# Performance work log

Hardware: AMD Instinct MI355X
Metric: run time of the kernel (lower is better)

Reference implementation:

```python
import jax, jax.numpy as jnp
import numpy as np

NEG_SLOPE = 0.2  # PyG GATConv default negative_slope
HEADS1, HID = 8, 256


def gat_conv(x, src, dst, W, att_src, att_dst, bias, heads, out_ch):
    """PyG-style GATConv: project, per-edge attention, segment softmax over dst, scatter-add."""
    N = x.shape[0]
    h = (x @ W.T).reshape(N, heads, out_ch)                 # [N,H,C]
    a_s = jnp.einsum('nhc,hc->nh', h, att_src)              # [N,H]
    a_d = jnp.einsum('nhc,hc->nh', h, att_dst)
    e = jax.nn.leaky_relu(a_s[src] + a_d[dst], NEG_SLOPE)   # [E,H]
    m = jax.ops.segment_max(e, dst, num_segments=N)         # stable softmax per dst node
    ex = jnp.exp(e - m[dst])
    denom = jax.ops.segment_sum(ex, dst, num_segments=N)
    alpha = ex / (denom[dst] + 1e-16)                       # [E,H]
    out = jax.ops.segment_sum(alpha[:, :, None] * h[src], dst, num_segments=N)  # [N,H,C]
    return out.reshape(N, heads * out_ch) + bias


def setup_inputs() -> dict:
    key = jax.random.key(0)
    ks = jax.random.split(key, 20)
    Nc, Ncol, E = 4000, 16000, 100000
    nf, cf, gain, hid, H, emb = 64, 128, 2, HID, HEADS1, 128
    s = 0.05
    return {
        'constraints_state': jax.random.normal(ks[0], (Nc, nf), jnp.float32),
        'columns_state':     jax.random.normal(ks[1], (Ncol, cf), jnp.float32),
        'edges':             jax.random.randint(ks[2], (2, E), 0, Nc + Ncol, jnp.int64),
        'W_node': jax.random.normal(ks[3], (hid, nf * gain), jnp.float32) * s,
        'b_node': jnp.zeros((hid,), jnp.float32),
        'W_col':  jax.random.normal(ks[4], (hid, cf * gain), jnp.float32) * s,
        'b_col':  jnp.zeros((hid,), jnp.float32),
        'W1':       jax.random.normal(ks[5], (H * hid, hid), jnp.float32) * s,
        'att_src1': jax.random.normal(ks[6], (H, hid), jnp.float32) * s,
        'att_dst1': jax.random.normal(ks[7], (H, hid), jnp.float32) * s,
        'b1':       jnp.zeros((H * hid,), jnp.float32),
        'W2':       jax.random.normal(ks[8], (hid, H * hid), jnp.float32) * s,
        'att_src2': jax.random.normal(ks[9], (1, hid), jnp.float32) * s,
        'att_dst2': jax.random.normal(ks[10], (1, hid), jnp.float32) * s,
        'b2':       jnp.zeros((hid,), jnp.float32),
        'W_out': jax.random.normal(ks[11], (emb, hid), jnp.float32) * s,
        'b_out': jnp.zeros((emb,), jnp.float32),
    }


def reference(constraints_state, columns_state, edges,
              W_node, b_node, W_col, b_col,
              W1, att_src1, att_dst1, b1,
              W2, att_src2, att_dst2, b2,
              W_out, b_out):
    gain = 2
    x_n = jnp.tile(constraints_state, (1, gain))
    x_c = jnp.tile(columns_state, (1, gain))
    h_n = jax.nn.relu(x_n @ W_node.T + b_node)
    h_c = jax.nn.relu(x_c @ W_col.T + b_col)
    x = jnp.concatenate([h_n, h_c], axis=0)                 # [N, hid]
    N = x.shape[0]
    loops = jnp.arange(N)
    # conv1: edges as given (+ self-loops, PyG default)
    src1 = jnp.concatenate([edges[0], loops])
    dst1 = jnp.concatenate([edges[1], loops])
    x = jax.nn.relu(gat_conv(x, src1, dst1, W1, att_src1, att_dst1, b1, HEADS1, HID))
    # conv2: flipped edges (+ self-loops), 1 head
    src2 = jnp.concatenate([edges[1], loops])
    dst2 = jnp.concatenate([edges[0], loops])
    x = jax.nn.relu(gat_conv(x, src2, dst2, W2, att_src2, att_dst2, b2, 1, HID))
    logits = x[-columns_state.shape[0]:] @ W_out.T + b_out  # [Ncol, embed_dim]
    return logits
```

## Files before the change

### kernel.cpp

```cpp
#include <hip/hip_runtime.h>


#define NEG_SLOPE 0.2f

typedef __attribute__((ext_vector_type(8))) short bf16x8;
typedef __attribute__((ext_vector_type(4))) float f32x4;

__device__ __forceinline__ float bf2f(unsigned short u) {
  return __uint_as_float(((unsigned)u) << 16);
}
__device__ __forceinline__ unsigned short f2bf(float f) {
  unsigned u = __float_as_uint(f);
  u += 0x7fffu + ((u >> 16) & 1u);
  return (unsigned short)(u >> 16);
}

__device__ __forceinline__ void async_copy16(const void* g, void* l) {
  __builtin_amdgcn_global_load_lds(
      (const __attribute__((address_space(1))) unsigned int*)g,
      (__attribute__((address_space(3))) unsigned int*)l, 16, 0, 0);
}

__global__ void prep(const float* __restrict__ Wn, const float* __restrict__ Wc,
                     const float* __restrict__ W1, const float* __restrict__ W2,
                     const float* __restrict__ Wout,
                     const float* __restrict__ cons, const float* __restrict__ cols,
                     const float* __restrict__ att_s1, const float* __restrict__ att_d1,
                     unsigned short* __restrict__ Wn_b, unsigned short* __restrict__ Wc_b,
                     unsigned short* __restrict__ W1b, unsigned short* __restrict__ W2b,
                     unsigned short* __restrict__ Woutb,
                     unsigned short* __restrict__ consb, unsigned short* __restrict__ colsb,
                     float* __restrict__ v_s1, float* __restrict__ v_d1,
                     int n_cons, int n_cols) {
  const int S0 = 256 * 64;
  const int S1 = 256 * 128;
  const int S2 = 2048 * 256;
  const int S3 = 256 * 2048;
  const int S4 = 128 * 256;
  const int S5 = 2048;
  int total = S0 + S1 + S2 + S3 + S4 + n_cons + n_cols + S5;
  for (int idx = blockIdx.x * 256 + threadIdx.x; idx < total; idx += gridDim.x * 256) {
    int i = idx;
    if (i < S0) { int o = i >> 6, j = i & 63;
      Wn_b[i] = f2bf(Wn[o * 128 + j] + Wn[o * 128 + 64 + j]); continue; }
    i -= S0;
    if (i < S1) { int o = i >> 7, j = i & 127;
      Wc_b[i] = f2bf(Wc[o * 256 + j] + Wc[o * 256 + 128 + j]); continue; }
    i -= S1;
    if (i < S2) { W1b[i] = f2bf(W1[i]); continue; }
    i -= S2;
    if (i < S3) { W2b[i] = f2bf(W2[i]); continue; }
    i -= S3;
    if (i < S4) { Woutb[i] = f2bf(Wout[i]); continue; }
    i -= S4;
    if (i < n_cons) { consb[i] = f2bf(cons[i]); continue; }
    i -= n_cons;
    if (i < n_cols) { colsb[i] = f2bf(cols[i]); continue; }
    i -= n_cols;
    {
      int h = i >> 8, k = i & 255;
      const float* Wrow = W1 + (size_t)h * 256 * 256 + k;
      const float* as = att_s1 + h * 256;
      const float* ad = att_d1 + h * 256;
      float s = 0.f, d = 0.f;
      for (int c = 0; c < 256; ++c) {
        float w = Wrow[(size_t)c * 256];
        s += as[c] * w;
        d += ad[c] * w;
      }
      v_s1[i] = s; v_d1[i] = d;
    }
  }
}

__global__ __launch_bounds__(256) void a1_dots(const unsigned short* __restrict__ xb,
                                               const float* __restrict__ v_s,
                                               const float* __restrict__ v_d,
                                               float* __restrict__ a_s,
                                               float* __restrict__ a_d, int N) {
  __shared__ float vs[2048], vd[2048];
  for (int i = threadIdx.x; i < 2048; i += 256) { vs[i] = v_s[i]; vd[i] = v_d[i]; }
  __syncthreads();
  int n = blockIdx.x * 256 + threadIdx.x;
  if (n >= N) return;
  const unsigned short* row = xb + (size_t)n * 256;
  float s[8] = {}, d[8] = {};
  for (int c = 0; c < 256; c += 8) {
    bf16x8 xv = *(const bf16x8*)(row + c);
    float xf[8];
#pragma unroll
    for (int i = 0; i < 8; ++i) xf[i] = bf2f(((const unsigned short*)&xv)[i]);
#pragma unroll
    for (int h = 0; h < 8; ++h)
#pragma unroll
      for (int i = 0; i < 8; ++i) {
        s[h] += xf[i] * vs[h * 256 + c + i];
        d[h] += xf[i] * vd[h * 256 + c + i];
      }
  }
#pragma unroll
  for (int h = 0; h < 8; ++h) { a_s[n * 8 + h] = s[h]; a_d[n * 8 + h] = d[h]; }
}

template <bool C_BF16, bool BIAS, bool RELU, bool BDIAG>
__global__ __launch_bounds__(512) void gemm_mfma_bt(const unsigned short* __restrict__ A,
                                                    const unsigned short* __restrict__ W,
                                                    const float* __restrict__ bias,
                                                    void* __restrict__ Cv,
                                                    int M, int K, int Nout, int lda) {
  __shared__ short smem[2 * 128 * 64];
  short* sA = smem;
  short* sB = smem + 128 * 64;
  float* Cf = (float*)Cv;
  unsigned short* Cb = (unsigned short*)Cv;

  const int tid = threadIdx.x;
  const int lane = tid & 63, w = tid >> 6;
  const int m0 = blockIdx.y * 128, n0 = blockIdx.x * 128;
  const int koff = BDIAG ? (n0 >> 8) << 8 : 0;
  const int wm = (w & 3) * 32, wn = (w >> 2) * 64;
  const int fr = lane & 15;
  const int frs = fr & 7;
  const int quad = lane >> 4;

  f32x4 acc[2][4];
#pragma unroll
  for (int i = 0; i < 2; ++i)
#pragma unroll
    for (int j = 0; j < 4; ++j) acc[i][j] = (f32x4){0.f, 0.f, 0.f, 0.f};

  for (int k0 = 0; k0 < K; k0 += 64) {
#pragma unroll
    for (int i = 0; i < 2; ++i) {
      int c = i * 512 + tid;
      int row = c >> 3, kc = c & 7;
      int kcs = kc ^ (row & 7);
      int grow = m0 + row;
      if (grow >= M) grow = M - 1;
      async_copy16(A + (size_t)grow * lda + koff + k0 + kcs * 8, &sA[(i * 512 + w * 64) * 8]);
    }
#pragma unroll
    for (int i = 0; i < 2; ++i) {
      int c = i * 512 + tid;
      int row = c >> 3, kc = c & 7;
      int kcs = kc ^ (row & 7);
      async_copy16(W + (size_t)(n0 + row) * K + k0 + kcs * 8, &sB[(i * 512 + w * 64) * 8]);
    }
    __syncthreads();

#pragma unroll
    for (int ks = 0; ks < 2; ++ks) {
      bf16x8 af[2], bfr[4];
#pragma unroll
      for (int mi = 0; mi < 2; ++mi) {
        int row = wm + mi * 16 + fr;
        af[mi] = *(const bf16x8*)&sA[(row * 8 + ((ks * 4 + quad) ^ frs)) * 8];
      }
#pragma unroll
      for (int ni = 0; ni < 4; ++ni) {
        int row = wn + ni * 16 + fr;
        bfr[ni] = *(const bf16x8*)&sB[(row * 8 + ((ks * 4 + quad) ^ frs)) * 8];
      }
#pragma unroll
      for (int mi = 0; mi < 2; ++mi)
#pragma unroll
        for (int ni = 0; ni < 4; ++ni)
          acc[mi][ni] = __builtin_amdgcn_mfma_f32_16x16x32_bf16(
              af[mi], bfr[ni], acc[mi][ni], 0, 0, 0);
    }
    __syncthreads();
  }

  if (C_BF16) {
    unsigned short* hsh = (unsigned short*)smem;
#pragma unroll
    for (int mi = 0; mi < 2; ++mi)
#pragma unroll
      for (int ni = 0; ni < 4; ++ni) {
        int col = wn + ni * 16 + fr;
        float bv = BIAS ? bias[n0 + col] : 0.f;
        f32x4 v = acc[mi][ni];
#pragma unroll
        for (int r = 0; r < 4; ++r) {
          int row = wm + mi * 16 + quad * 4 + r;
          float x = v[r] + bv;
          if (RELU) x = fmaxf(x, 0.f);
          hsh[row * 128 + (col ^ (((row >> 2) & 3) << 5))] = f2bf(x);
        }
      }
    __syncthreads();
#pragma unroll
    for (int i = 0; i < 4; ++i) {
      int slot = i * 512 + tid;
      int row = slot >> 4, cg = slot & 15;
      int colbase = cg * 8;
      bf16x8 val = *(const bf16x8*)&hsh[row * 128 + (colbase ^ (((row >> 2) & 3) << 5))];
      int grow = m0 + row;
      if (grow < M)
        *(bf16x8*)(Cb + (size_t)grow * Nout + n0 + colbase) = val;
    }
  } else {
#pragma unroll
    for (int mi = 0; mi < 2; ++mi)
#pragma unroll
      for (int ni = 0; ni < 4; ++ni) {
        int col = n0 + wn + ni * 16 + fr;
        float bv = BIAS ? bias[col] : 0.f;
        f32x4 v = acc[mi][ni];
#pragma unroll
        for (int r = 0; r < 4; ++r) {
          int row = m0 + wm + mi * 16 + quad * 4 + r;
          if (row < M) {
            float x = v[r] + bv;
            if (RELU) x = fmaxf(x, 0.f);
            Cf[(size_t)row * Nout + col] = x;
          }
        }
      }
  }
}

__global__ __launch_bounds__(512) void gemm_mfma_k2048(const unsigned short* __restrict__ A,
                                                       const unsigned short* __restrict__ W,
                                                       unsigned short* __restrict__ C,
                                                       const float* __restrict__ att_s,
                                                       const float* __restrict__ att_d,
                                                       float* __restrict__ a_s,
                                                       float* __restrict__ a_d,
                                                       int M, int K) {
  __shared__ short sA[32 * 64];
  __shared__ short sB[256 * 64];
  const int tid = threadIdx.x;
  const int lane = tid & 63, w = tid >> 6;
  const int m0 = blockIdx.x * 32;
  const int fr = lane & 15, quad = lane >> 4;
  const int frs = fr & 7;

  f32x4 acc[2][2];
#pragma unroll
  for (int i = 0; i < 2; ++i)
#pragma unroll
    for (int j = 0; j < 2; ++j) acc[i][j] = (f32x4){0.f, 0.f, 0.f, 0.f};

  for (int k0 = 0; k0 < K; k0 += 64) {
    if (w < 4) {
      int row = tid >> 3, kc = tid & 7;
      int kcs = kc ^ (row & 7);
      int grow = m0 + row;
      if (grow >= M) grow = M - 1;
      async_copy16(A + (size_t)grow * K + k0 + kcs * 8, &sA[(w * 64) * 8]);
    }
#pragma unroll
    for (int i = 0; i < 4; ++i) {
      int c = i * 512 + tid;
      int row = c >> 3, kc = c & 7;
      int kcs = kc ^ (row & 7);
      async_copy16(W + (size_t)row * K + k0 + kcs * 8, &sB[(i * 512 + w * 64) * 8]);
    }
    __syncthreads();

#pragma unroll
    for (int ks = 0; ks < 2; ++ks) {
      bf16x8 af[2], bfr[2];
#pragma unroll
      for (int mi = 0; mi < 2; ++mi) {
        int row = mi * 16 + fr;
        af[mi] = *(const bf16x8*)&sA[(row * 8 + ((ks * 4 + quad) ^ frs)) * 8];
      }
#pragma unroll
      for (int ni = 0; ni < 2; ++ni) {
        int row = w * 32 + ni * 16 + fr;
        bfr[ni] = *(const bf16x8*)&sB[(row * 8 + ((ks * 4 + quad) ^ frs)) * 8];
      }
#pragma unroll
      for (int mi = 0; mi < 2; ++mi)
#pragma unroll
        for (int ni = 0; ni < 2; ++ni)
          acc[mi][ni] = __builtin_amdgcn_mfma_f32_16x16x32_bf16(
              af[mi], bfr[ni], acc[mi][ni], 0, 0, 0);
    }
    __syncthreads();
  }

  unsigned short* hsh = (unsigned short*)sB;
#pragma unroll
  for (int mi = 0; mi < 2; ++mi)
#pragma unroll
    for (int ni = 0; ni < 2; ++ni) {
      int col = w * 32 + ni * 16 + fr;
      f32x4 v = acc[mi][ni];
#pragma unroll
      for (int r = 0; r < 4; ++r) {
        int rl = mi * 16 + quad * 4 + r;
        hsh[rl * 256 + col] = f2bf(v[r]);
      }
    }
  __syncthreads();

#pragma unroll
  for (int i = 0; i < 2; ++i) {
    int slot = i * 512 + tid;
    int row = slot >> 5, cg = slot & 31;
    int grow = m0 + row;
    if (grow < M)
      *(bf16x8*)(C + (size_t)grow * 256 + cg * 8) = *(const bf16x8*)&hsh[row * 256 + cg * 8];
  }

  int r = tid >> 4;
  int cbase = (tid & 15) * 16;
  float s = 0.f, d = 0.f;
#pragma unroll
  for (int q = 0; q < 2; ++q) {
    bf16x8 hv8 = *(const bf16x8*)&hsh[r * 256 + cbase + q * 8];
    const unsigned short* hp = (const unsigned short*)&hv8;
#pragma unroll
    for (int i = 0; i < 8; ++i) {
      int c = cbase + q * 8 + i;
      float hv = bf2f(hp[i]);
      s += hv * att_s[c];
      d += hv * att_d[c];
    }
  }
#pragma unroll
  for (int off = 8; off; off >>= 1) {
    s += __shfl_down(s, off);
    d += __shfl_down(d, off);
  }
  if ((tid & 15) == 0 && m0 + r < M) {
    a_s[m0 + r] = s;
    a_d[m0 + r] = d;
  }
}

__global__ void build_count(const void* __restrict__ edges_raw, int E, int N,
                            int* __restrict__ esrc, int* __restrict__ edst,
                            int* __restrict__ cnt1, int* __restrict__ cnt2, int E1) {
  const long long* p64 = (const long long*)edges_raw;
  const int* p32 = (const int*)edges_raw;
  bool is64 = true;
#pragma unroll
  for (int i = 0; i < 8; ++i) {
    long long v = p64[i];
    if (v < 0 || v >= N) is64 = false;
  }
  int idx = blockIdx.x * 256 + threadIdx.x;
  if (idx >= E1) return;
  int s, d;
  if (idx < E) {
    if (is64) { s = (int)p64[idx]; d = (int)p64[E + idx]; }
    else      { s = p32[idx];      d = p32[E + idx]; }
  } else {
    s = d = idx - E;
  }
  esrc[idx] = s;
  edst[idx] = d;
  atomicAdd(&cnt1[d], 1);
  atomicAdd(&cnt2[s], 1);
}

__device__ __forceinline__ void scan_one(const int* __restrict__ cnt,
                                         int* __restrict__ indptr,
                                         int* __restrict__ cur, int N, int* buf) {
  int t = threadIdx.x, lane = t & 63, w = t >> 6;
  int running = 0;
  for (int base = 0; base < N; base += 1024) {
    int v = (base + t < N) ? cnt[base + t] : 0;
    int incl = v;
#pragma unroll
    for (int off = 1; off < 64; off <<= 1) {
      int y = __shfl_up(incl, off);
      if (lane >= off) incl += y;
    }
    if (lane == 63) buf[w] = incl;
    __syncthreads();
    if (t < 16) {
      int x = buf[t];
#pragma unroll
      for (int off = 1; off < 16; off <<= 1) {
        int y = __shfl_up(x, off);
        if (t >= off) x += y;
      }
      buf[t] = x;
    }
    __syncthreads();
    int woff = w ? buf[w - 1] : 0;
    int tot = buf[15];
    if (base + t < N) {
      int excl = running + woff + incl - v;
      indptr[base + t] = excl;
      cur[base + t] = excl;
    }
    running += tot;
    __syncthreads();
  }
  if (t == 0) indptr[N] = running;
  __syncthreads();
}

__global__ __launch_bounds__(1024) void scan2_kernel(const int* cnt1, int* indptr1, int* cur1,
                                                     const int* cnt2, int* indptr2, int* cur2,
                                                     int N) {
  __shared__ int buf[16];
  scan_one(cnt1, indptr1, cur1, N, buf);
  scan_one(cnt2, indptr2, cur2, N, buf);
}

__global__ void scatter_edges(const int* __restrict__ esrc, const int* __restrict__ edst,
                              int* __restrict__ cur1, int* __restrict__ cur2,
                              int* __restrict__ nbr1, int* __restrict__ nbr2, int E1) {
  int e = blockIdx.x * 256 + threadIdx.x;
  if (e >= E1) return;
  int s = esrc[e], d = edst[e];
  int p1 = atomicAdd(&cur1[d], 1);
  nbr1[p1] = s;
  int p2 = atomicAdd(&cur2[s], 1);
  nbr2[p2] = d;
}

__global__ __launch_bounds__(256) void alpha1_kernel(const float* __restrict__ a_s,
                                                     const float* __restrict__ a_d,
                                                     const int* __restrict__ indptr,
                                                     const int* __restrict__ nbr,
                                                     float* __restrict__ alpha, int N) {
  int n = blockIdx.x * 256 + threadIdx.x;
  if (n >= N) return;
  int start = indptr[n], end = indptr[n + 1];
  float ad[8];
  *(float4*)&ad[0] = *(const float4*)&a_d[n * 8];
  *(float4*)&ad[4] = *(const float4*)&a_d[n * 8 + 4];
  float m[8], ssum[8];
#pragma unroll
  for (int h = 0; h < 8; ++h) { m[h] = -1e30f; ssum[h] = 0.f; }
  for (int p = start; p < end; ++p) {
    int s = nbr[p];
    float as[8];
    *(float4*)&as[0] = *(const float4*)&a_s[s * 8];
    *(float4*)&as[4] = *(const float4*)&a_s[s * 8 + 4];
#pragma unroll
    for (int h = 0; h < 8; ++h) {
      float e = as[h] + ad[h];
      e = e > 0.f ? e : NEG_SLOPE * e;
      float nm = fmaxf(m[h], e);
      ssum[h] = ssum[h] * __expf(m[h] - nm) + __expf(e - nm);
      m[h] = nm;
    }
  }
  float inv[8];
#pragma unroll
  for (int h = 0; h < 8; ++h) inv[h] = 1.f / (ssum[h] + 1e-16f);
  for (int p = start; p < end; ++p) {
    int s = nbr[p];
    float as[8];
    *(float4*)&as[0] = *(const float4*)&a_s[s * 8];
    *(float4*)&as[4] = *(const float4*)&a_s[s * 8 + 4];
    float av[8];
#pragma unroll
    for (int h = 0; h < 8; ++h) {
      float e = as[h] + ad[h];
      e = e > 0.f ? e : NEG_SLOPE * e;
      av[h] = __expf(e - m[h]) * inv[h];
    }
    *(float4*)&alpha[(size_t)p * 8] = *(const float4*)&av[0];
    *(float4*)&alpha[(size_t)p * 8 + 4] = *(const float4*)&av[4];
  }
}

__global__ __launch_bounds__(256) void alpha2_kernel(const float* __restrict__ a_s,
                                                     const float* __restrict__ a_d,
                                                     const int* __restrict__ indptr,
                                                     const int* __restrict__ nbr,
                                                     float* __restrict__ alpha,
                                                     int Nc, int Ncol) {
  int i = blockIdx.x * 256 + threadIdx.x;
  if (i >= Ncol) return;
  int n = Nc + i;
  int start = indptr[n], end = indptr[n + 1];
  float ad = a_d[n];
  float m = -1e30f, ssum = 0.f;
  for (int p = start; p < end; ++p) {
    float e = a_s[nbr[p]] + ad;
    e = e > 0.f ? e : NEG_SLOPE * e;
    float nm = fmaxf(m, e);
    ssum = ssum * __expf(m - nm) + __expf(e - nm);
    m = nm;
  }
  float inv = 1.f / (ssum + 1e-16f);
  for (int p = start; p < end; ++p) {
    float e = a_s[nbr[p]] + ad;
    e = e > 0.f ? e : NEG_SLOPE * e;
    alpha[p] = __expf(e - m) * inv;
  }
}

__global__ __launch_bounds__(256) void agg1_kernel(const unsigned short* __restrict__ xb,
                                                   const float* __restrict__ alpha,
                                                   const int* __restrict__ indptr,
                                                   const int* __restrict__ nbr,
                                                   unsigned short* __restrict__ agg,
                                                   int N) {
  __shared__ float al_sh[4][64 * 8];
  const int w = threadIdx.x >> 6, lane = threadIdx.x & 63;
  const int dst = blockIdx.x * 4 + w;
  if (dst >= N) return;
  const int start = indptr[dst];
  const int deg = indptr[dst + 1] - start;
  const int c0 = lane * 4;

  float acc[8][4];
#pragma unroll
  for (int h = 0; h < 8; ++h)
#pragma unroll
    for (int i = 0; i < 4; ++i) acc[h][i] = 0.f;

  for (int base = 0; base < deg; base += 64) {
    int cnt = min(64, deg - base);
    int s = 0;
    if (lane < cnt) {
      int slot = start + base + lane;
      s = nbr[slot];
      f32x4 a0 = *(const f32x4*)&alpha[(size_t)slot * 8];
      f32x4 a1 = *(const f32x4*)&alpha[(size_t)slot * 8 + 4];
      *(f32x4*)&al_sh[w][lane * 8] = a0;
      *(f32x4*)&al_sh[w][lane * 8 + 4] = a1;
    }
    __builtin_amdgcn_wave_barrier();
    for (int j = 0; j < cnt; ++j) {
      int sj = __shfl(s, j);
      f32x4 alo = *(const f32x4*)&al_sh[w][j * 8];
      f32x4 ahi = *(const f32x4*)&al_sh[w][j * 8 + 4];
      ushort4 xv = *(const ushort4*)(xb + (size_t)sj * 256 + c0);
      float x0 = bf2f(xv.x), x1 = bf2f(xv.y), x2 = bf2f(xv.z), x3 = bf2f(xv.w);
#pragma unroll
      for (int h = 0; h < 4; ++h) {
        acc[h][0] += alo[h] * x0; acc[h][1] += alo[h] * x1;
        acc[h][2] += alo[h] * x2; acc[h][3] += alo[h] * x3;
      }
#pragma unroll
      for (int h = 0; h < 4; ++h) {
        acc[h + 4][0] += ahi[h] * x0; acc[h + 4][1] += ahi[h] * x1;
        acc[h + 4][2] += ahi[h] * x2; acc[h + 4][3] += ahi[h] * x3;
      }
    }
    __builtin_amdgcn_wave_barrier();
  }

  unsigned short* op = agg + (size_t)dst * 2048;
#pragma unroll
  for (int h = 0; h < 8; ++h) {
    unsigned short ov[4];
#pragma unroll
    for (int i = 0; i < 4; ++i) ov[i] = f2bf(acc[h][i]);
    *((ushort4*)(op + h * 256 + c0)) = *((const ushort4*)ov);
  }
}

__global__ __launch_bounds__(256) void agg2_kernel(const unsigned short* __restrict__ h2,
                                                   const float* __restrict__ alpha,
                                                   const int* __restrict__ indptr,
                                                   const int* __restrict__ nbr,
                                                   const float* __restrict__ b2,
                                                   unsigned short* __restrict__ x3,
                                                   int Nc, int Ncol) {
  const int w = threadIdx.x >> 6, lane = threadIdx.x & 63;
  const int i0 = blockIdx.x * 4 + w;
  if (i0 >= Ncol) return;
  const int dst = Nc + i0;
  const int start = indptr[dst];
  const int deg = indptr[dst + 1] - start;
  const int c0 = lane * 4;
  float acc[4] = {0.f, 0.f, 0.f, 0.f};

  for (int base = 0; base < deg; base += 64) {
    int cnt = min(64, deg - base);
    int s = 0; float a = 0.f;
    if (lane < cnt) {
      int slot = start + base + lane;
      s = nbr[slot];
      a = alpha[slot];
    }
    for (int j = 0; j < cnt; ++j) {
      int sj = __shfl(s, j);
      float al = __shfl(a, j);
      ushort4 hv = *(const ushort4*)(h2 + (size_t)sj * 256 + c0);
      acc[0] += al * bf2f(hv.x);
      acc[1] += al * bf2f(hv.y);
      acc[2] += al * bf2f(hv.z);
      acc[3] += al * bf2f(hv.w);
    }
  }

  float4 bv = *(const float4*)&b2[c0];
  unsigned short ov[4];
  ov[0] = f2bf(fmaxf(acc[0] + bv.x, 0.f));
  ov[1] = f2bf(fmaxf(acc[1] + bv.y, 0.f));
  ov[2] = f2bf(fmaxf(acc[2] + bv.z, 0.f));
  ov[3] = f2bf(fmaxf(acc[3] + bv.w, 0.f));
  *((ushort4*)(x3 + (size_t)i0 * 256 + c0)) = *((const ushort4*)ov);
}

extern "C" void kernel_launch(void* const* d_in, const int* in_sizes, int n_in,
                              void* d_out, int out_size, void* d_ws, size_t ws_size,
                              hipStream_t stream) {
  (void)n_in; (void)out_size; (void)ws_size;
  const float* constraints = (const float*)d_in[0];
  const float* columns     = (const float*)d_in[1];
  const void*  edges       = d_in[2];
  const float* W_node = (const float*)d_in[3];
  const float* b_node = (const float*)d_in[4];
  const float* W_col  = (const float*)d_in[5];
  const float* b_col  = (const float*)d_in[6];
  const float* W1       = (const float*)d_in[7];
  const float* att_src1 = (const float*)d_in[8];
  const float* att_dst1 = (const float*)d_in[9];
  const float* b1       = (const float*)d_in[10];
  const float* W2       = (const float*)d_in[11];
  const float* att_src2 = (const float*)d_in[12];
  const float* att_dst2 = (const float*)d_in[13];
  const float* b2       = (const float*)d_in[14];
  const float* W_out    = (const float*)d_in[15];
  const float* b_out    = (const float*)d_in[16];

  const int Nc   = in_sizes[0] / 64;
  const int Ncol = in_sizes[1] / 128;
  const int E    = in_sizes[2] / 2;
  const int N    = Nc + Ncol;
  const int E1   = E + N;

  char* p = (char*)d_ws;
  size_t off = 0;
  auto alloc = [&](size_t nbytes) -> void* {
    void* r = p + off;
    off = (off + nbytes + 255) & ~(size_t)255;
    return r;
  };
  unsigned short* Wn_b  = (unsigned short*)alloc(2ull * 256 * 64);
  unsigned short* Wc_b  = (unsigned short*)alloc(2ull * 256 * 128);
  unsigned short* W1b   = (unsigned short*)alloc(2ull * 2048 * 256);
  unsigned short* W2b   = (unsigned short*)alloc(2ull * 256 * 2048);
  unsigned short* Woutb = (unsigned short*)alloc(2ull * 128 * 256);
  unsigned short* consb = (unsigned short*)alloc(2ull * (size_t)Nc * 64);
  unsigned short* colsb = (unsigned short*)alloc(2ull * (size_t)Ncol * 128);
  unsigned short* xb    = (unsigned short*)alloc(2ull * (size_t)N * 256);
  float* v_s1 = (float*)alloc(sizeof(float) * 8 * 256);
  float* v_d1 = (float*)alloc(sizeof(float) * 8 * 256);
  float* a_s1 = (float*)alloc(sizeof(float) * (size_t)N * 8);
  float* a_d1 = (float*)alloc(sizeof(float) * (size_t)N * 8);
  int* esrc = (int*)alloc(4ull * E1);
  int* edst = (int*)alloc(4ull * E1);
  int* cnt1 = (int*)alloc(4ull * 2 * N);
  int* cnt2 = cnt1 + N;
  int* indptr1 = (int*)alloc(4ull * (N + 1));
  int* cur1    = (int*)alloc(4ull * N);
  int* indptr2 = (int*)alloc(4ull * (N + 1));
  int* cur2    = (int*)alloc(4ull * N);
  int* nbr1 = (int*)alloc(4ull * E1);
  int* nbr2 = (int*)alloc(4ull * E1);
  float* alpha1 = (float*)alloc(sizeof(float) * 8ull * E1);
  float* alpha2 = (float*)alloc(sizeof(float) * (size_t)E1);
  unsigned short* agg = (unsigned short*)alloc(2ull * (size_t)N * 2048);
  unsigned short* x2  = (unsigned short*)alloc(2ull * (size_t)N * 2048);
  unsigned short* h2b = (unsigned short*)alloc(2ull * (size_t)N * 256);
  float* a_s2 = (float*)alloc(sizeof(float) * (size_t)N);
  float* a_d2 = (float*)alloc(sizeof(float) * (size_t)N);
  unsigned short* x3 = (unsigned short*)alloc(2ull * (size_t)Ncol * 256);

  hipMemsetAsync(cnt1, 0, 4ull * 2 * N, stream);
  prep<<<1024, 256, 0, stream>>>(W_node, W_col, W1, W2, W_out, constraints, columns,
                                 att_src1, att_dst1,
                                 Wn_b, Wc_b, W1b, W2b, Woutb, consb, colsb,
                                 v_s1, v_d1, Nc * 64, Ncol * 128);

  gemm_mfma_bt<true, true, true, false><<<dim3(2, (Nc + 127) / 128), 512, 0, stream>>>(
      consb, Wn_b, b_node, xb, Nc, 64, 256, 64);
  gemm_mfma_bt<true, true, true, false><<<dim3(2, (Ncol + 127) / 128), 512, 0, stream>>>(
      colsb, Wc_b, b_col, xb + (size_t)Nc * 256, Ncol, 128, 256, 128);

  a1_dots<<<(N + 255) / 256, 256, 0, stream>>>(xb, v_s1, v_d1, a_s1, a_d1, N);

  build_count<<<(E1 + 255) / 256, 256, 0, stream>>>(edges, E, N, esrc, edst, cnt1, cnt2, E1);
  scan2_kernel<<<1, 1024, 0, stream>>>(cnt1, indptr1, cur1, cnt2, indptr2, cur2, N);
  scatter_edges<<<(E1 + 255) / 256, 256, 0, stream>>>(esrc, edst, cur1, cur2, nbr1, nbr2, E1);

  alpha1_kernel<<<(N + 255) / 256, 256, 0, stream>>>(a_s1, a_d1, indptr1, nbr1, alpha1, N);
  agg1_kernel<<<(N + 3) / 4, 256, 0, stream>>>(xb, alpha1, indptr1, nbr1, agg, N);
  gemm_mfma_bt<true, true, true, true><<<dim3(16, (N + 127) / 128), 512, 0, stream>>>(
      agg, W1b, b1, x2, N, 256, 2048, 2048);

  gemm_mfma_k2048<<<(N + 31) / 32, 512, 0, stream>>>(
      x2, W2b, h2b, att_src2, att_dst2, a_s2, a_d2, N, 2048);
  alpha2_kernel<<<(Ncol + 255) / 256, 256, 0, stream>>>(a_s2, a_d2, indptr2, nbr2, alpha2,
                                                        Nc, Ncol);
  agg2_kernel<<<(Ncol + 3) / 4, 256, 0, stream>>>(h2b, alpha2, indptr2, nbr2, b2, x3,
                                                  Nc, Ncol);

  gemm_mfma_bt<false, true, false, false><<<dim3(1, (Ncol + 127) / 128), 512, 0, stream>>>(
      x3, Woutb, b_out, (float*)d_out, Ncol, 256, 128, 256);
}
```

Measured before the change: 375.9 us.

## Double-buffer conv2 GEMM, split N across blocks, fuse alpha2 softmax into aggregation

```diff
diff --git a/kernel.cpp b/kernel.cpp
--- a/kernel.cpp
+++ b/kernel.cpp
@@ -220,115 +220,113 @@
   }
 }
 
-__global__ __launch_bounds__(512) void gemm_mfma_k2048(const unsigned short* __restrict__ A,
-                                                       const unsigned short* __restrict__ W,
-                                                       unsigned short* __restrict__ C,
-                                                       const float* __restrict__ att_s,
-                                                       const float* __restrict__ att_d,
-                                                       float* __restrict__ a_s,
-                                                       float* __restrict__ a_d,
-                                                       int M, int K) {
-  __shared__ short sA[32 * 64];
-  __shared__ short sB[256 * 64];
+__global__ __launch_bounds__(512) void gemm_k2048_db(const unsigned short* __restrict__ A,
+                                                     const unsigned short* __restrict__ W,
+                                                     unsigned short* __restrict__ C,
+                                                     const float* __restrict__ att_s,
+                                                     const float* __restrict__ att_d,
+                                                     float* __restrict__ a_s,
+                                                     float* __restrict__ a_d,
+                                                     int M, int K) {
+  __shared__ short sA[2][32 * 64];
+  __shared__ short sB[2][128 * 64];
   const int tid = threadIdx.x;
   const int lane = tid & 63, w = tid >> 6;
-  const int m0 = blockIdx.x * 32;
+  const int m0 = blockIdx.y * 32;
+  const int n0 = blockIdx.x * 128;
   const int fr = lane & 15, quad = lane >> 4;
   const int frs = fr & 7;
-
-  f32x4 acc[2][2];
-#pragma unroll
-  for (int i = 0; i < 2; ++i)
-#pragma unroll
-    for (int j = 0; j < 2; ++j) acc[i][j] = (f32x4){0.f, 0.f, 0.f, 0.f};
-
-  for (int k0 = 0; k0 < K; k0 += 64) {
-    if (w < 4) {
-      int row = tid >> 3, kc = tid & 7;
-      int kcs = kc ^ (row & 7);
-      int grow = m0 + row;
-      if (grow >= M) grow = M - 1;
-      async_copy16(A + (size_t)grow * K + k0 + kcs * 8, &sA[(w * 64) * 8]);
-    }
-#pragma unroll
-    for (int i = 0; i < 4; ++i) {
-      int c = i * 512 + tid;
-      int row = c >> 3, kc = c & 7;
-      int kcs = kc ^ (row & 7);
-      async_copy16(W + (size_t)row * K + k0 + kcs * 8, &sB[(i * 512 + w * 64) * 8]);
-    }
-    __syncthreads();
-
+  const int wn = w * 16;
+  const int NT = K >> 6;
+
+  const int arow = tid >> 3;
+  const int akc = (tid & 7) ^ (arow & 7);
+  int aclamp = m0 + arow; if (aclamp >= M) aclamp = M - 1;
+
+  f32x4 acc0 = (f32x4){0.f, 0.f, 0.f, 0.f};
+  f32x4 acc1 = (f32x4){0.f, 0.f, 0.f, 0.f};
+
+#define STAGE(KT, BUF)                                                         \
+  do {                                                                         \
+    int k0_ = (KT) << 6;                                                       \
+    if (w < 4)                                                                 \
+      async_copy16(A + (size_t)aclamp * K + k0_ + akc * 8,                     \
+                   &sA[BUF][(w * 64) * 8]);                                    \
+    _Pragma("unroll")                                                          \
+    for (int i_ = 0; i_ < 2; ++i_) {                                           \
+      int c_ = i_ * 512 + tid;                                                 \
+      int row_ = c_ >> 3, kc_ = (c_ & 7) ^ (row_ & 7);                         \
+      async_copy16(W + (size_t)(n0 + row_) * K + k0_ + kc_ * 8,                \
+                   &sB[BUF][(i_ * 512 + w * 64) * 8]);                         \
+    }                                                                          \
+  } while (0)
+
+  STAGE(0, 0);
+  for (int kt = 0; kt < NT; ++kt) {
+    int cur = kt & 1;
+    if (kt + 1 < NT) {
+      STAGE(kt + 1, cur ^ 1);
+      if (w < 4) __builtin_amdgcn_s_waitcnt(0x0F73);
+      else       __builtin_amdgcn_s_waitcnt(0x0F72);
+    } else {
+      __builtin_amdgcn_s_waitcnt(0x0F70);
+    }
+    __builtin_amdgcn_s_barrier();
 #pragma unroll
     for (int ks = 0; ks < 2; ++ks) {
-      bf16x8 af[2], bfr[2];
-#pragma unroll
-      for (int mi = 0; mi < 2; ++mi) {
-        int row = mi * 16 + fr;
-        af[mi] = *(const bf16x8*)&sA[(row * 8 + ((ks * 4 + quad) ^ frs)) * 8];
-      }
-#pragma unroll
-      for (int ni = 0; ni < 2; ++ni) {
-        int row = w * 32 + ni * 16 + fr;
-        bfr[ni] = *(const bf16x8*)&sB[(row * 8 + ((ks * 4 + quad) ^ frs)) * 8];
-      }
-#pragma unroll
-      for (int mi = 0; mi < 2; ++mi)
-#pragma unroll
-        for (int ni = 0; ni < 2; ++ni)
-          acc[mi][ni] = __builtin_amdgcn_mfma_f32_16x16x32_bf16(
-              af[mi], bfr[ni], acc[mi][ni], 0, 0, 0);
-    }
-    __syncthreads();
-  }
-
-  unsigned short* hsh = (unsigned short*)sB;
-#pragma unroll
-  for (int mi = 0; mi < 2; ++mi)
-#pragma unroll
-    for (int ni = 0; ni < 2; ++ni) {
-      int col = w * 32 + ni * 16 + fr;
-      f32x4 v = acc[mi][ni];
-#pragma unroll
-      for (int r = 0; r < 4; ++r) {
-        int rl = mi * 16 + quad * 4 + r;
-        hsh[rl * 256 + col] = f2bf(v[r]);
-      }
-    }
+      int sw = (ks * 4 + quad) ^ frs;
+      bf16x8 af0 = *(const bf16x8*)&sA[cur][((fr) * 8 + sw) * 8];
+      bf16x8 af1 = *(const bf16x8*)&sA[cur][((16 + fr) * 8 + sw) * 8];
+      bf16x8 bf0 = *(const bf16x8*)&sB[cur][((wn + fr) * 8 + sw) * 8];
+      acc0 = __builtin_amdgcn_mfma_f32_16x16x32_bf16(af0, bf0, acc0, 0, 0, 0);
+      acc1 = __builtin_amdgcn_mfma_f32_16x16x32_bf16(af1, bf0, acc1, 0, 0, 0);
+    }
+    __builtin_amdgcn_s_waitcnt(0xC07F);
+    __builtin_amdgcn_s_barrier();
+  }
+#undef STAGE
+
+  unsigned short* hsh = (unsigned short*)sA;
+#pragma unroll
+  for (int mi = 0; mi < 2; ++mi) {
+    f32x4 v = mi ? acc1 : acc0;
+    int col = wn + fr;
+#pragma unroll
+    for (int r = 0; r < 4; ++r) {
+      int row = mi * 16 + quad * 4 + r;
+      hsh[row * 128 + col] = f2bf(v[r]);
+    }
+  }
   __syncthreads();
 
-#pragma unroll
-  for (int i = 0; i < 2; ++i) {
-    int slot = i * 512 + tid;
-    int row = slot >> 5, cg = slot & 31;
+  {
+    int row = tid >> 4, cg = tid & 15;
     int grow = m0 + row;
     if (grow < M)
-      *(bf16x8*)(C + (size_t)grow * 256 + cg * 8) = *(const bf16x8*)&hsh[row * 256 + cg * 8];
-  }
-
-  int r = tid >> 4;
-  int cbase = (tid & 15) * 16;
-  float s = 0.f, d = 0.f;
-#pragma unroll
-  for (int q = 0; q < 2; ++q) {
-    bf16x8 hv8 = *(const bf16x8*)&hsh[r * 256 + cbase + q * 8];
+      *(bf16x8*)(C + (size_t)grow * 256 + n0 + cg * 8) =
+          *(const bf16x8*)&hsh[row * 128 + cg * 8];
+  }
+  {
+    int r = tid >> 4;
+    int cb = (tid & 15) * 8;
+    bf16x8 hv8 = *(const bf16x8*)&hsh[r * 128 + cb];
     const unsigned short* hp = (const unsigned short*)&hv8;
+    float s = 0.f, d = 0.f;
 #pragma unroll
     for (int i = 0; i < 8; ++i) {
-      int c = cbase + q * 8 + i;
       float hv = bf2f(hp[i]);
-      s += hv * att_s[c];
-      d += hv * att_d[c];
-    }
-  }
-#pragma unroll
-  for (int off = 8; off; off >>= 1) {
-    s += __shfl_down(s, off);
-    d += __shfl_down(d, off);
-  }
-  if ((tid & 15) == 0 && m0 + r < M) {
-    a_s[m0 + r] = s;
-    a_d[m0 + r] = d;
+      s += hv * att_s[n0 + cb + i];
+      d += hv * att_d[n0 + cb + i];
+    }
+#pragma unroll
+    for (int off = 8; off; off >>= 1) {
+      s += __shfl_down(s, off);
+      d += __shfl_down(d, off);
+    }
+    if ((tid & 15) == 0 && m0 + r < M) {
+      atomicAdd(&a_s[m0 + r], s);
+      atomicAdd(&a_d[m0 + r], d);
+    }
   }
 }
 
@@ -462,33 +460,6 @@
     }
     *(float4*)&alpha[(size_t)p * 8] = *(const float4*)&av[0];
     *(float4*)&alpha[(size_t)p * 8 + 4] = *(const float4*)&av[4];
-  }
-}
-
-__global__ __launch_bounds__(256) void alpha2_kernel(const float* __restrict__ a_s,
-                                                     const float* __restrict__ a_d,
-                                                     const int* __restrict__ indptr,
-                                                     const int* __restrict__ nbr,
-                                                     float* __restrict__ alpha,
-                                                     int Nc, int Ncol) {
-  int i = blockIdx.x * 256 + threadIdx.x;
-  if (i >= Ncol) return;
-  int n = Nc + i;
-  int start = indptr[n], end = indptr[n + 1];
-  float ad = a_d[n];
-  float m = -1e30f, ssum = 0.f;
-  for (int p = start; p < end; ++p) {
-    float e = a_s[nbr[p]] + ad;
-    e = e > 0.f ? e : NEG_SLOPE * e;
-    float nm = fmaxf(m, e);
-    ssum = ssum * __expf(m - nm) + __expf(e - nm);
-    m = nm;
-  }
-  float inv = 1.f / (ssum + 1e-16f);
-  for (int p = start; p < end; ++p) {
-    float e = a_s[nbr[p]] + ad;
-    e = e > 0.f ? e : NEG_SLOPE * e;
-    alpha[p] = __expf(e - m) * inv;
   }
 }
 
@@ -554,33 +525,50 @@
   }
 }
 
-__global__ __launch_bounds__(256) void agg2_kernel(const unsigned short* __restrict__ h2,
-                                                   const float* __restrict__ alpha,
-                                                   const int* __restrict__ indptr,
-                                                   const int* __restrict__ nbr,
-                                                   const float* __restrict__ b2,
-                                                   unsigned short* __restrict__ x3,
-                                                   int Nc, int Ncol) {
+__global__ __launch_bounds__(256) void agg2_fused(const unsigned short* __restrict__ h2,
+                                                  const float* __restrict__ a_s,
+                                                  const float* __restrict__ a_d,
+                                                  const int* __restrict__ indptr,
+                                                  const int* __restrict__ nbr,
+                                                  const float* __restrict__ b2,
+                                                  unsigned short* __restrict__ x3,
+                                                  int Nc, int Ncol) {
   const int w = threadIdx.x >> 6, lane = threadIdx.x & 63;
   const int i0 = blockIdx.x * 4 + w;
   if (i0 >= Ncol) return;
   const int dst = Nc + i0;
   const int start = indptr[dst];
   const int deg = indptr[dst + 1] - start;
+  const float ad = a_d[dst];
+  float run_m = -1e30f, run_s = 0.f;
+  float acc[4] = {0.f, 0.f, 0.f, 0.f};
   const int c0 = lane * 4;
-  float acc[4] = {0.f, 0.f, 0.f, 0.f};
 
   for (int base = 0; base < deg; base += 64) {
     int cnt = min(64, deg - base);
-    int s = 0; float a = 0.f;
+    float ev = -1e30f;
+    int s = 0;
     if (lane < cnt) {
-      int slot = start + base + lane;
-      s = nbr[slot];
-      a = alpha[slot];
-    }
+      s = nbr[start + base + lane];
+      float e = a_s[s] + ad;
+      ev = e > 0.f ? e : NEG_SLOPE * e;
+    }
+    float cm = ev;
+#pragma unroll
+    for (int off = 32; off; off >>= 1) cm = fmaxf(cm, __shfl_xor(cm, off));
+    float nm = fmaxf(run_m, cm);
+    float sc = __expf(run_m - nm);
+    float e = (lane < cnt) ? __expf(ev - nm) : 0.f;
+    float cs = e;
+#pragma unroll
+    for (int off = 32; off; off >>= 1) cs += __shfl_xor(cs, off);
+    run_s = run_s * sc + cs;
+    run_m = nm;
+#pragma unroll
+    for (int i = 0; i < 4; ++i) acc[i] *= sc;
     for (int j = 0; j < cnt; ++j) {
       int sj = __shfl(s, j);
-      float al = __shfl(a, j);
+      float al = __shfl(e, j);
       ushort4 hv = *(const ushort4*)(h2 + (size_t)sj * 256 + c0);
       acc[0] += al * bf2f(hv.x);
       acc[1] += al * bf2f(hv.y);
@@ -589,12 +577,13 @@
     }
   }
 
+  float inv = 1.f / (run_s + 1e-16f);
   float4 bv = *(const float4*)&b2[c0];
   unsigned short ov[4];
-  ov[0] = f2bf(fmaxf(acc[0] + bv.x, 0.f));
-  ov[1] = f2bf(fmaxf(acc[1] + bv.y, 0.f));
-  ov[2] = f2bf(fmaxf(acc[2] + bv.z, 0.f));
-  ov[3] = f2bf(fmaxf(acc[3] + bv.w, 0.f));
+  ov[0] = f2bf(fmaxf(acc[0] * inv + bv.x, 0.f));
+  ov[1] = f2bf(fmaxf(acc[1] * inv + bv.y, 0.f));
+  ov[2] = f2bf(fmaxf(acc[2] * inv + bv.z, 0.f));
+  ov[3] = f2bf(fmaxf(acc[3] * inv + bv.w, 0.f));
   *((ushort4*)(x3 + (size_t)i0 * 256 + c0)) = *((const ushort4*)ov);
 }
 
@@ -656,15 +645,16 @@
   int* nbr1 = (int*)alloc(4ull * E1);
   int* nbr2 = (int*)alloc(4ull * E1);
   float* alpha1 = (float*)alloc(sizeof(float) * 8ull * E1);
-  float* alpha2 = (float*)alloc(sizeof(float) * (size_t)E1);
   unsigned short* agg = (unsigned short*)alloc(2ull * (size_t)N * 2048);
   unsigned short* x2  = (unsigned short*)alloc(2ull * (size_t)N * 2048);
   unsigned short* h2b = (unsigned short*)alloc(2ull * (size_t)N * 256);
-  float* a_s2 = (float*)alloc(sizeof(float) * (size_t)N);
-  float* a_d2 = (float*)alloc(sizeof(float) * (size_t)N);
+  float* a2buf = (float*)alloc(sizeof(float) * 2ull * N);
+  float* a_s2 = a2buf;
+  float* a_d2 = a2buf + N;
   unsigned short* x3 = (unsigned short*)alloc(2ull * (size_t)Ncol * 256);
 
   hipMemsetAsync(cnt1, 0, 4ull * 2 * N, stream);
+  hipMemsetAsync(a2buf, 0, sizeof(float) * 2ull * N, stream);
   prep<<<1024, 256, 0, stream>>>(W_node, W_col, W1, W2, W_out, constraints, columns,
                                  att_src1, att_dst1,
                                  Wn_b, Wc_b, W1b, W2b, Woutb, consb, colsb,
@@ -686,12 +676,10 @@
   gemm_mfma_bt<true, true, true, true><<<dim3(16, (N + 127) / 128), 512, 0, stream>>>(
       agg, W1b, b1, x2, N, 256, 2048, 2048);
 
-  gemm_mfma_k2048<<<(N + 31) / 32, 512, 0, stream>>>(
+  gemm_k2048_db<<<dim3(2, (N + 31) / 32), 512, 0, stream>>>(
       x2, W2b, h2b, att_src2, att_dst2, a_s2, a_d2, N, 2048);
-  alpha2_kernel<<<(Ncol + 255) / 256, 256, 0, stream>>>(a_s2, a_d2, indptr2, nbr2, alpha2,
-                                                        Nc, Ncol);
-  agg2_kernel<<<(Ncol + 3) / 4, 256, 0, stream>>>(h2b, alpha2, indptr2, nbr2, b2, x3,
-                                                  Nc, Ncol);
+  agg2_fused<<<(Ncol + 3) / 4, 256, 0, stream>>>(h2b, a_s2, a_d2, indptr2, nbr2, b2, x3,
+                                                 Nc, Ncol);
 
   gemm_mfma_bt<false, true, false, false><<<dim3(1, (Ncol + 127) / 128), 512, 0, stream>>>(
       x3, Woutb, b_out, (float*)d_out, Ncol, 256, 128, 256);
```

New measurement: 380.8 us. About the same (+1.3%).
